# Performance work log

Measured on AMD Instinct MI355X. Metric: run time of the kernel, lower is better.

The kernel has to match this reference:

```python
import jax, jax.numpy as jnp
import numpy as np

EMBED_DIM = 256
MIN_SCALE = 0.5
BASE = 100.0
NDIM = 3
EPS = 1e-5


def basis_norm(psi, w):
    # w: [B, N] float weights; reduce over token dim (-2)
    norm_sq = jnp.sum(w[..., None] * (psi * psi), axis=-2, keepdims=True)
    return psi / jnp.sqrt(norm_sq + EPS)


def rotary(f, coords, lift):
    # lift: [D//2, 3]; phase: [B, N, D//2]
    phase = coords @ lift.T
    c, s = jnp.cos(phase), jnp.sin(phase)
    f1, f2 = jnp.split(f, 2, axis=-1)
    return jnp.concatenate([f1 * c - f2 * s, f1 * s + f2 * c], axis=-1)


def setup_inputs() -> dict:
    key = jax.random.key(0)
    ks = jax.random.split(key, 12)
    B, N, D = 4, 8192, EMBED_DIM
    phi = jax.random.normal(ks[0], (B, N, D), dtype=jnp.float32)
    coords = jax.random.normal(ks[1], (B, N, NDIM), dtype=jnp.float32)
    weights = jax.random.uniform(ks[2], (B, N), dtype=jnp.float32)
    scale = 1.0 / np.sqrt(D)
    Wq = jax.random.normal(ks[3], (D, D), dtype=jnp.float32) * scale
    bq = jnp.zeros((D,), dtype=jnp.float32)
    Wk = jax.random.normal(ks[4], (D, D), dtype=jnp.float32) * scale
    bk = jax.random.normal(ks[5], (D,), dtype=jnp.float32) * 0.01
    Wv = jax.random.normal(ks[6], (D, D), dtype=jnp.float32) * scale
    bv = jax.random.normal(ks[7], (D,), dtype=jnp.float32) * 0.01
    Wo = jax.random.normal(ks[8], (D, D), dtype=jnp.float32) * scale
    bo = jnp.zeros((D,), dtype=jnp.float32)
    # rotary lift init: k_norms * random unit vecs
    half = D // 2
    scales = BASE ** (-2.0 * np.arange(half) / D)
    k_norms = (2.0 * np.pi / MIN_SCALE) * scales  # [half]
    u = np.asarray(jax.random.normal(ks[9], (half, NDIM)))
    u = u / np.linalg.norm(u, axis=-1, keepdims=True)
    lift = jnp.asarray(k_norms[:, None] * u, dtype=jnp.float32)  # [half, 3]
    return {"phi": phi, "coords": coords, "weights": weights,
            "Wq": Wq, "bq": bq, "Wk": Wk, "bk": bk, "Wv": Wv, "bv": bv,
            "Wo": Wo, "bo": bo, "lift": lift}


def reference(phi, coords, weights, Wq, bq, Wk, bk, Wv, bv, Wo, bo, lift):
    q = phi @ Wq.T + bq
    k = basis_norm(phi @ Wk.T + bk, weights)
    v = basis_norm(phi @ Wv.T + bv, weights)
    q = rotary(q, coords, lift)
    k = rotary(k, coords, lift)
    k = k * weights[..., None]  # float-weights branch
    kv = jnp.einsum('bnd,bne->bde', k, v)   # [B, D, D]
    out = jnp.einsum('bnd,bde->bne', q, kv)  # [B, N, D]
    return out @ Wo.T + bo
```

## Files before the change

### kernel.cpp

```cpp
#include <hip/hip_runtime.h>
#include <hip/hip_bf16.h>
#include <stdint.h>

#define DEV __device__ __forceinline__

typedef short short8 __attribute__((ext_vector_type(8)));
typedef float floatx4 __attribute__((ext_vector_type(4)));
typedef uint32_t uint32x4 __attribute__((ext_vector_type(4)));

constexpr int D = 256;
constexpr int NTOK = 8192;
constexpr int MTOT = 4 * NTOK;

DEV void gl_lds16(const void* g, void* l) {
  __builtin_amdgcn_global_load_lds(
      (const __attribute__((address_space(1))) void*)g,
      (__attribute__((address_space(3))) void*)l, 16, 0, 0);
}

DEV float bflo(uint32_t u) { return __uint_as_float(u << 16); }
DEV float bfhi(uint32_t u) { return __uint_as_float(u & 0xffff0000u); }
DEV uint32_t packbf(float a, float b) {
  uint16_t xa = __builtin_bit_cast(uint16_t, __float2bfloat16(a));
  uint16_t xb = __builtin_bit_cast(uint16_t, __float2bfloat16(b));
  return (uint32_t)xa | ((uint32_t)xb << 16);
}

constexpr int PHI_E = MTOT * D;
constexpr int W_E = D * D;
__global__ __launch_bounds__(256) void convert(
    const float* __restrict__ phi, const float* __restrict__ Wq,
    const float* __restrict__ Wk, const float* __restrict__ Wv,
    uint32_t* __restrict__ dst, float2* __restrict__ nszero) {
  if (blockIdx.x == 0) {
    const float2 z = {0.f, 0.f};
#pragma unroll
    for (int k = 0; k < 4; k++) nszero[k * 256 + threadIdx.x] = z;
  }
  const int idx2 = blockIdx.x * 256 + threadIdx.x;
  const int e0 = idx2 * 2;
  float2 v;
  if (e0 < PHI_E) {
    v = ((const float2*)phi)[idx2];
  } else {
    int r = e0 - PHI_E;
    if (r < W_E) v = ((const float2*)Wq)[r >> 1];
    else if (r < 2 * W_E) v = ((const float2*)Wk)[(r - W_E) >> 1];
    else v = ((const float2*)Wv)[(r - 2 * W_E) >> 1];
  }
  dst[idx2] = packbf(v.x, v.y);
}

__global__ __launch_bounds__(256, 2) void gemm_qkv(
    const __hip_bfloat16* __restrict__ phi,
    const __hip_bfloat16* __restrict__ W16,
    const float* __restrict__ bq, const float* __restrict__ bk, const float* __restrict__ bv,
    const float* __restrict__ coords, const float* __restrict__ wts,
    const float* __restrict__ lift,
    __hip_bfloat16* __restrict__ Qb, __hip_bfloat16* __restrict__ Kb,
    __hip_bfloat16* __restrict__ Vb, float* __restrict__ nsk, float* __restrict__ nsv) {
  __shared__ __align__(16) char As[8192];
  __shared__ __align__(16) char Bs[16384];
  const int t = threadIdx.x, lane = t & 63, wid = t >> 6;
  const int wm = (wid & 1) * 64, wn = (wid >> 1) * 64;
  const int l16 = lane & 15, q4 = lane >> 4;
  const int m0 = blockIdx.x * 128;
  const int mat = blockIdx.y;
  const __hip_bfloat16* W = W16 + (size_t)mat * W_E;
  const float* bias = (mat == 0) ? bq : (mat == 1) ? bk : bv;
  __hip_bfloat16* Out = (mat == 0) ? Qb : (mat == 1) ? Kb : Vb;

  floatx4 acc[4][8] = {};

  const int srow = wid * 16 + (lane >> 2);
  const int skoff = (lane & 3) * 8;
  const __hip_bfloat16* gA = phi + (size_t)(m0 + srow) * D + skoff;
  const __hip_bfloat16* gB = W + (size_t)srow * D + skoff;
  char* lA = As + srow * 64 + skoff * 2;
  char* lB = Bs + srow * 64 + skoff * 2;

  for (int kt = 0; kt < 256; kt += 32) {
    gl_lds16(gA + kt, lA);
    gl_lds16(gA + kt + 64 * D, lA + 4096);
    gl_lds16(gB + kt, lB);
    gl_lds16(gB + kt + 64 * D, lB + 4096);
    gl_lds16(gB + kt + 128 * D, lB + 8192);
    gl_lds16(gB + kt + 192 * D, lB + 12288);
    __syncthreads();
    short8 af[4], bf8[8];
#pragma unroll
    for (int i = 0; i < 4; i++)
      af[i] = *(const short8*)(As + (wm + i * 16 + l16) * 64 + q4 * 16);
#pragma unroll
    for (int j = 0; j < 8; j++) {
      const int col = wn + (j & 3) * 16 + (j >> 2) * 128 + l16;
      bf8[j] = *(const short8*)(Bs + col * 64 + q4 * 16);
    }
#pragma unroll
    for (int i = 0; i < 4; i++)
#pragma unroll
      for (int j = 0; j < 8; j++)
        acc[i][j] = __builtin_amdgcn_mfma_f32_16x16x32_bf16(af[i], bf8[j], acc[i][j], 0, 0, 0);
    __syncthreads();
  }

  float bcol[8];
#pragma unroll
  for (int j = 0; j < 8; j++)
    bcol[j] = bias[wn + (j & 3) * 16 + (j >> 2) * 128 + l16];

  if (mat == 0) {
    float lx[4], ly[4], lz[4];
#pragma unroll
    for (int jj = 0; jj < 4; jj++) {
      const int c = wn + jj * 16 + l16;
      lx[jj] = lift[c * 3 + 0]; ly[jj] = lift[c * 3 + 1]; lz[jj] = lift[c * 3 + 2];
    }
#pragma unroll
    for (int i = 0; i < 4; i++) {
#pragma unroll
      for (int r = 0; r < 4; r++) {
        const int row = m0 + wm + i * 16 + q4 * 4 + r;
        const float cx = coords[row * 3 + 0];
        const float cy = coords[row * 3 + 1];
        const float cz = coords[row * 3 + 2];
#pragma unroll
        for (int jj = 0; jj < 4; jj++) {
          const int c = wn + jj * 16 + l16;
          const float p = cx * lx[jj] + cy * ly[jj] + cz * lz[jj];
          float s, cs;
          __sincosf(p, &s, &cs);
          const float f1 = acc[i][jj][r] + bcol[jj];
          const float f2 = acc[i][jj + 4][r] + bcol[jj + 4];
          Out[(size_t)row * D + c]       = __float2bfloat16(f1 * cs - f2 * s);
          Out[(size_t)row * D + c + 128] = __float2bfloat16(f1 * s + f2 * cs);
        }
      }
    }
  } else {
    const int b = m0 >> 13;
    float* ns = (mat == 1) ? nsk : nsv;
    float colsum[8] = {};
#pragma unroll
    for (int i = 0; i < 4; i++) {
#pragma unroll
      for (int r = 0; r < 4; r++) {
        const int row = m0 + wm + i * 16 + q4 * 4 + r;
        const float w = wts[row];
#pragma unroll
        for (int j = 0; j < 8; j++) {
          const int col = wn + (j & 3) * 16 + (j >> 2) * 128 + l16;
          const float psi = acc[i][j][r] + bcol[j];
          Out[(size_t)row * D + col] = __float2bfloat16(psi);
          colsum[j] += w * psi * psi;
        }
      }
    }
#pragma unroll
    for (int j = 0; j < 8; j++) {
      float s = colsum[j];
      s += __shfl_xor(s, 16);
      s += __shfl_xor(s, 32);
      if (q4 == 0) {
        const int col = wn + (j & 3) * 16 + (j >> 2) * 128 + l16;
        atomicAdd(&ns[b * D + col], s);
      }
    }
  }
}

__global__ __launch_bounds__(256, 2) void vproj_pk(
    const __hip_bfloat16* __restrict__ Vb, const float* __restrict__ Wo,
    const float* __restrict__ nsv, __hip_bfloat16* __restrict__ vproj,
    __hip_bfloat16* __restrict__ Kb, const float* __restrict__ coords,
    const float* __restrict__ wts, const float* __restrict__ lift,
    const float* __restrict__ nsk) {
  __shared__ __align__(16) char As[8192];
  __shared__ __align__(16) char Bs[8192];
  __shared__ __align__(16) float isv[256];
  const int bx = blockIdx.x;
  const int t = threadIdx.x;

  if (bx < 512) {
    const int lane = t & 63, wid = t >> 6;
    const int wm = (wid & 1) * 64, wn = (wid >> 1) * 64;
    const int l16 = lane & 15, q4 = lane >> 4;
    const int m0 = (bx >> 1) * 128, n0 = (bx & 1) * 128;
    const int b = m0 >> 13;
    isv[t] = rsqrtf(nsv[b * D + t] + 1e-5f);
    __syncthreads();
    floatx4 acc[4][4] = {};
    const int srow = wid * 16 + (lane >> 2);
    const int skoff = (lane & 3) * 8;
    const __hip_bfloat16* gA = Vb + (size_t)(m0 + srow) * D + skoff;
    const float* gB0 = Wo + (size_t)(n0 + srow) * D + skoff;
    const float* gB1 = Wo + (size_t)(n0 + srow + 64) * D + skoff;
    char* lA = As + srow * 64 + skoff * 2;
    char* lB = Bs + srow * 64 + skoff * 2;
    for (int kt = 0; kt < 256; kt += 32) {
      gl_lds16(gA + kt, lA);
      gl_lds16(gA + kt + 64 * D, lA + 4096);
      const float4 w0 = *(const float4*)(gB0 + kt);
      const float4 w1 = *(const float4*)(gB0 + kt + 4);
      const float4 w2 = *(const float4*)(gB1 + kt);
      const float4 w3 = *(const float4*)(gB1 + kt + 4);
      const float4 i0 = *(const float4*)(&isv[kt + skoff]);
      const float4 i1 = *(const float4*)(&isv[kt + skoff + 4]);
      uint32x4 p0, p1;
      p0[0] = packbf(w0.x * i0.x, w0.y * i0.y);
      p0[1] = packbf(w0.z * i0.z, w0.w * i0.w);
      p0[2] = packbf(w1.x * i1.x, w1.y * i1.y);
      p0[3] = packbf(w1.z * i1.z, w1.w * i1.w);
      p1[0] = packbf(w2.x * i0.x, w2.y * i0.y);
      p1[1] = packbf(w2.z * i0.z, w2.w * i0.w);
      p1[2] = packbf(w3.x * i1.x, w3.y * i1.y);
      p1[3] = packbf(w3.z * i1.z, w3.w * i1.w);
      *(uint32x4*)lB = p0;
      *(uint32x4*)(lB + 4096) = p1;
      __syncthreads();
      short8 af[4], bf8[4];
#pragma unroll
      for (int i = 0; i < 4; i++) {
        af[i]  = *(const short8*)(As + (wm + i * 16 + l16) * 64 + q4 * 16);
        bf8[i] = *(const short8*)(Bs + (wn + i * 16 + l16) * 64 + q4 * 16);
      }
#pragma unroll
      for (int i = 0; i < 4; i++)
#pragma unroll
        for (int j = 0; j < 4; j++)
          acc[i][j] = __builtin_amdgcn_mfma_f32_16x16x32_bf16(af[i], bf8[j], acc[i][j], 0, 0, 0);
      __syncthreads();
    }
#pragma unroll
    for (int j = 0; j < 4; j++) {
      const int colg = n0 + wn + j * 16 + l16;
#pragma unroll
      for (int i = 0; i < 4; i++) {
        const int rowg = m0 + wm + i * 16 + q4 * 4;
#pragma unroll
        for (int r = 0; r < 4; r++)
          vproj[(size_t)(rowg + r) * D + colg] = __float2bfloat16(acc[i][j][r]);
      }
    }
  } else {
    const int j = t & 63, rloc = t >> 6;
    const int pb = bx - 512;
    const int r0 = pb * 256;
    const int b = r0 >> 13;
    const int j0 = 2 * j, j1 = 2 * j + 1;
    const float lx0 = lift[j0 * 3 + 0], ly0 = lift[j0 * 3 + 1], lz0 = lift[j0 * 3 + 2];
    const float lx1 = lift[j1 * 3 + 0], ly1 = lift[j1 * 3 + 1], lz1 = lift[j1 * 3 + 2];
    const int nb = b * D;
    const float ik0 = rsqrtf(nsk[nb + j0] + 1e-5f);
    const float ik1 = rsqrtf(nsk[nb + j1] + 1e-5f);
    const float ik2 = rsqrtf(nsk[nb + 128 + j0] + 1e-5f);
    const float ik3 = rsqrtf(nsk[nb + 128 + j1] + 1e-5f);
    uint32_t* K32 = (uint32_t*)Kb;
    for (int it = 0; it < 64; it++) {
      const size_t row = (size_t)r0 + it * 4 + rloc;
      const float cx = coords[row * 3 + 0];
      const float cy = coords[row * 3 + 1];
      const float cz = coords[row * 3 + 2];
      const float p0 = cx * lx0 + cy * ly0 + cz * lz0;
      const float p1 = cx * lx1 + cy * ly1 + cz * lz1;
      float s0, c0, s1, c1;
      __sincosf(p0, &s0, &c0);
      __sincosf(p1, &s1, &c1);
      const float w = wts[row];
      const size_t base = row * 128;
      const uint32_t klo = K32[base + j], khi = K32[base + 64 + j];
      const float k1a = bflo(klo) * ik0, k1b = bfhi(klo) * ik1;
      const float k2a = bflo(khi) * ik2, k2b = bfhi(khi) * ik3;
      K32[base + j]      = packbf((k1a * c0 - k2a * s0) * w, (k1b * c1 - k2b * s1) * w);
      K32[base + 64 + j] = packbf((k1a * s0 + k2a * c0) * w, (k1b * s1 + k2b * c1) * w);
    }
  }
}

__global__ __launch_bounds__(256, 2) void gemm_tn(
    const __hip_bfloat16* __restrict__ Vp, const __hip_bfloat16* __restrict__ Kwb,
    __hip_bfloat16* __restrict__ part) {
  __shared__ __align__(16) char Asm[128 * 80];
  __shared__ __align__(16) char Bsm[128 * 80];
  const int t = threadIdx.x, lane = t & 63, wid = t >> 6;
  const int wm = (wid & 1) * 64, wn = (wid >> 1) * 64;
  const int l16 = lane & 15, q4 = lane >> 4;
  const int chunk = blockIdx.x, ed = blockIdx.y, b = blockIdx.z;
  const int e0 = (ed & 1) * 128, d0 = (ed >> 1) * 128;
  const uint32_t* V32 = (const uint32_t*)Vp;
  const uint32_t* K32 = (const uint32_t*)Kwb;
  const int s_np = (((t & 3) | ((t >> 6) << 2)) ^ ((t >> 4) & 3));
  const int s_e2lo = (t >> 2) & 15;
  floatx4 acc[4][4] = {};
  for (int nt = 0; nt < 256; nt += 32) {
    const int nbase = chunk * 256 + nt;
    const size_t tokbase = ((size_t)b * NTOK + nbase + 2 * s_np) * 128;
#pragma unroll
    for (int r = 0; r < 4; r++) {
      const int e2 = s_e2lo + r * 16;
      {
        const uint32_t a0 = V32[tokbase + (e0 >> 1) + e2];
        const uint32_t a1 = V32[tokbase + 128 + (e0 >> 1) + e2];
        *(uint32_t*)(Asm + (2 * e2) * 80 + 4 * s_np)     = (a0 & 0xffffu) | (a1 << 16);
        *(uint32_t*)(Asm + (2 * e2 + 1) * 80 + 4 * s_np) = (a0 >> 16) | (a1 & 0xffff0000u);
      }
      {
        const uint32_t b0 = K32[tokbase + (d0 >> 1) + e2];
        const uint32_t b1 = K32[tokbase + 128 + (d0 >> 1) + e2];
        *(uint32_t*)(Bsm + (2 * e2) * 80 + 4 * s_np)     = (b0 & 0xffffu) | (b1 << 16);
        *(uint32_t*)(Bsm + (2 * e2 + 1) * 80 + 4 * s_np) = (b0 >> 16) | (b1 & 0xffff0000u);
      }
    }
    __syncthreads();
    short8 af[4], bf8[4];
#pragma unroll
    for (int i = 0; i < 4; i++) {
      af[i]  = *(const short8*)(Asm + (wm + i * 16 + l16) * 80 + q4 * 16);
      bf8[i] = *(const short8*)(Bsm + (wn + i * 16 + l16) * 80 + q4 * 16);
    }
#pragma unroll
    for (int i = 0; i < 4; i++)
#pragma unroll
      for (int j = 0; j < 4; j++)
        acc[i][j] = __builtin_amdgcn_mfma_f32_16x16x32_bf16(af[i], bf8[j], acc[i][j], 0, 0, 0);
    __syncthreads();
  }
  __hip_bfloat16* pt = part + (((size_t)(chunk * 4 + b)) << 16);
#pragma unroll
  for (int i = 0; i < 4; i++) {
#pragma unroll
    for (int r = 0; r < 4; r++) {
      const int eg = e0 + wm + i * 16 + q4 * 4 + r;
#pragma unroll
      for (int j = 0; j < 4; j++) {
        const int dg = d0 + wn + j * 16 + l16;
        pt[eg * 256 + dg] = __float2bfloat16(acc[i][j][r]);
      }
    }
  }
}

__global__ __launch_bounds__(256) void reduce_kvt(const uint32_t* __restrict__ part,
                                                  uint32_t* __restrict__ P) {
  const int flat2 = blockIdx.x * 256 + threadIdx.x;
  const int b = flat2 >> 15;
  const int off = flat2 & 32767;
  float sx = 0, sy = 0;
#pragma unroll
  for (int c = 0; c < 32; c++) {
    const uint32_t u = part[(((size_t)(c * 4 + b)) << 15) + off];
    sx += bflo(u); sy += bfhi(u);
  }
  P[flat2] = packbf(sx, sy);
}

__global__ __launch_bounds__(256, 2) void gemm_out(
    const __hip_bfloat16* __restrict__ A, const __hip_bfloat16* __restrict__ Pm,
    const float* __restrict__ bo, float* __restrict__ Og) {
  __shared__ __align__(16) char As[8192];
  __shared__ __align__(16) char Bs[8192];
  const int t = threadIdx.x, lane = t & 63, wid = t >> 6;
  const int wm = (wid & 1) * 64, wn = (wid >> 1) * 64;
  const int l16 = lane & 15, q4 = lane >> 4;
  const int m0 = blockIdx.x * 128, n0 = blockIdx.y * 128;
  const int b = m0 >> 13;
  const __hip_bfloat16* W = Pm + ((size_t)b << 16);
  floatx4 acc[4][4] = {};
  const int srow = wid * 16 + (lane >> 2);
  const int skoff = (lane & 3) * 8;
  const __hip_bfloat16* gA = A + (size_t)(m0 + srow) * D + skoff;
  const __hip_bfloat16* gB = W + (size_t)(n0 + srow) * D + skoff;
  char* lA = As + srow * 64 + skoff * 2;
  char* lB = Bs + srow * 64 + skoff * 2;
  for (int kt = 0; kt < 256; kt += 32) {
    gl_lds16(gA + kt, lA);
    gl_lds16(gA + kt + 64 * D, lA + 4096);
    gl_lds16(gB + kt, lB);
    gl_lds16(gB + kt + 64 * D, lB + 4096);
    __syncthreads();
    short8 af[4], bf8[4];
#pragma unroll
    for (int i = 0; i < 4; i++) {
      af[i]  = *(const short8*)(As + (wm + i * 16 + l16) * 64 + q4 * 16);
      bf8[i] = *(const short8*)(Bs + (wn + i * 16 + l16) * 64 + q4 * 16);
    }
#pragma unroll
    for (int i = 0; i < 4; i++)
#pragma unroll
      for (int j = 0; j < 4; j++)
        acc[i][j] = __builtin_amdgcn_mfma_f32_16x16x32_bf16(af[i], bf8[j], acc[i][j], 0, 0, 0);
    __syncthreads();
  }
#pragma unroll
  for (int j = 0; j < 4; j++) {
    const int colg = n0 + wn + j * 16 + l16;
    const float bb = bo[colg];
#pragma unroll
    for (int i = 0; i < 4; i++) {
      const int rowg = m0 + wm + i * 16 + q4 * 4;
#pragma unroll
      for (int r = 0; r < 4; r++)
        Og[(size_t)(rowg + r) * D + colg] = acc[i][j][r] + bb;
    }
  }
}

extern "C" void kernel_launch(void* const* d_in, const int* in_sizes, int n_in,
                              void* d_out, int out_size, void* d_ws, size_t ws_size,
                              hipStream_t stream) {
  const float* phi    = (const float*)d_in[0];
  const float* coords = (const float*)d_in[1];
  const float* wts    = (const float*)d_in[2];
  const float* bq     = (const float*)d_in[4];
  const float* bk     = (const float*)d_in[6];
  const float* bv     = (const float*)d_in[8];
  const float* Wo     = (const float*)d_in[9];
  const float* bo     = (const float*)d_in[10];
  const float* lift   = (const float*)d_in[11];

  char* ws = (char*)d_ws;
  __hip_bfloat16* phi16 = (__hip_bfloat16*)ws;
  __hip_bfloat16* W16   = (__hip_bfloat16*)(ws + 16777216);
  const size_t QOFF = 17170432;
  const size_t SZ = (size_t)MTOT * D * 2;
  __hip_bfloat16* Qb = (__hip_bfloat16*)(ws + QOFF);
  __hip_bfloat16* Kb = (__hip_bfloat16*)(ws + QOFF + SZ);
  __hip_bfloat16* Vb = (__hip_bfloat16*)(ws + QOFF + 2 * SZ);
  const size_t NOFF = QOFF + 3 * SZ;
  float* nsk = (float*)(ws + NOFF);
  float* nsv = (float*)(ws + NOFF + 4096);
  __hip_bfloat16* part = (__hip_bfloat16*)(ws + NOFF + 8192);
  __hip_bfloat16* P = (__hip_bfloat16*)(ws + NOFF + 8192 + 16777216);
  __hip_bfloat16* vproj = (__hip_bfloat16*)(ws + NOFF + 8192 + 16777216 + 524288);

  convert<<<16768, 256, 0, stream>>>(phi, (const float*)d_in[3], (const float*)d_in[5],
                                     (const float*)d_in[7], (uint32_t*)ws, (float2*)(ws + NOFF));
  gemm_qkv<<<dim3(256, 3), 256, 0, stream>>>(phi16, W16, bq, bk, bv, coords, wts, lift,
                                             Qb, Kb, Vb, nsk, nsv);
  vproj_pk<<<640, 256, 0, stream>>>(Vb, Wo, nsv, vproj, Kb, coords, wts, lift, nsk);
  gemm_tn<<<dim3(32, 4, 4), 256, 0, stream>>>(vproj, Kb, part);
  reduce_kvt<<<512, 256, 0, stream>>>((const uint32_t*)part, (uint32_t*)P);
  gemm_out<<<dim3(256, 2), 256, 0, stream>>>(Qb, P, bo, (float*)d_out);
}
```

Before: 191.6 us.

## Reassociate Wo into small per-batch KV matrix instead of projecting V per token

Drops the per-token V·Wo projection over all 32K tokens and instead computes the 256x256 KV matrix from raw V, folding the V normalisation into the reduction. A small per-batch GEMM then multiplies Wo into KV, and Wo is converted to bf16 in the existing convert kernel. The K rotary pass becomes its own kernel, and the qkv and tn GEMMs remap block IDs to group blocks across XCDs. This removes a large token-dimension GEMM in exchange for one extra tiny launch and a different rounding order.

```diff
diff --git a/kernel.cpp b/kernel.cpp
--- a/kernel.cpp
+++ b/kernel.cpp
@@ -6,7 +6,6 @@
 
 typedef short short8 __attribute__((ext_vector_type(8)));
 typedef float floatx4 __attribute__((ext_vector_type(4)));
-typedef uint32_t uint32x4 __attribute__((ext_vector_type(4)));
 
 constexpr int D = 256;
 constexpr int NTOK = 8192;
@@ -31,6 +30,7 @@
 __global__ __launch_bounds__(256) void convert(
     const float* __restrict__ phi, const float* __restrict__ Wq,
     const float* __restrict__ Wk, const float* __restrict__ Wv,
+    const float* __restrict__ Wo,
     uint32_t* __restrict__ dst, float2* __restrict__ nszero) {
   if (blockIdx.x == 0) {
     const float2 z = {0.f, 0.f};
@@ -46,7 +46,8 @@
     int r = e0 - PHI_E;
     if (r < W_E) v = ((const float2*)Wq)[r >> 1];
     else if (r < 2 * W_E) v = ((const float2*)Wk)[(r - W_E) >> 1];
-    else v = ((const float2*)Wv)[(r - 2 * W_E) >> 1];
+    else if (r < 3 * W_E) v = ((const float2*)Wv)[(r - 2 * W_E) >> 1];
+    else v = ((const float2*)Wo)[(r - 3 * W_E) >> 1];
   }
   dst[idx2] = packbf(v.x, v.y);
 }
@@ -64,8 +65,10 @@
   const int t = threadIdx.x, lane = t & 63, wid = t >> 6;
   const int wm = (wid & 1) * 64, wn = (wid >> 1) * 64;
   const int l16 = lane & 15, q4 = lane >> 4;
-  const int m0 = blockIdx.x * 128;
-  const int mat = blockIdx.y;
+  const int bid = blockIdx.x;
+  const int g = (bid & 7) * 96 + (bid >> 3);
+  const int mat = g % 3;
+  const int m0 = (g / 3) * 128;
   const __hip_bfloat16* W = W16 + (size_t)mat * W_E;
   const float* bias = (mat == 0) ? bq : (mat == 1) ? bk : bv;
   __hip_bfloat16* Out = (mat == 0) ? Qb : (mat == 1) ? Kb : Vb;
@@ -169,126 +172,58 @@
   }
 }
 
-__global__ __launch_bounds__(256, 2) void vproj_pk(
-    const __hip_bfloat16* __restrict__ Vb, const float* __restrict__ Wo,
-    const float* __restrict__ nsv, __hip_bfloat16* __restrict__ vproj,
+__global__ __launch_bounds__(256) void kpoint(
     __hip_bfloat16* __restrict__ Kb, const float* __restrict__ coords,
     const float* __restrict__ wts, const float* __restrict__ lift,
     const float* __restrict__ nsk) {
-  __shared__ __align__(16) char As[8192];
-  __shared__ __align__(16) char Bs[8192];
-  __shared__ __align__(16) float isv[256];
-  const int bx = blockIdx.x;
   const int t = threadIdx.x;
-
-  if (bx < 512) {
-    const int lane = t & 63, wid = t >> 6;
-    const int wm = (wid & 1) * 64, wn = (wid >> 1) * 64;
-    const int l16 = lane & 15, q4 = lane >> 4;
-    const int m0 = (bx >> 1) * 128, n0 = (bx & 1) * 128;
-    const int b = m0 >> 13;
-    isv[t] = rsqrtf(nsv[b * D + t] + 1e-5f);
-    __syncthreads();
-    floatx4 acc[4][4] = {};
-    const int srow = wid * 16 + (lane >> 2);
-    const int skoff = (lane & 3) * 8;
-    const __hip_bfloat16* gA = Vb + (size_t)(m0 + srow) * D + skoff;
-    const float* gB0 = Wo + (size_t)(n0 + srow) * D + skoff;
-    const float* gB1 = Wo + (size_t)(n0 + srow + 64) * D + skoff;
-    char* lA = As + srow * 64 + skoff * 2;
-    char* lB = Bs + srow * 64 + skoff * 2;
-    for (int kt = 0; kt < 256; kt += 32) {
-      gl_lds16(gA + kt, lA);
-      gl_lds16(gA + kt + 64 * D, lA + 4096);
-      const float4 w0 = *(const float4*)(gB0 + kt);
-      const float4 w1 = *(const float4*)(gB0 + kt + 4);
-      const float4 w2 = *(const float4*)(gB1 + kt);
-      const float4 w3 = *(const float4*)(gB1 + kt + 4);
-      const float4 i0 = *(const float4*)(&isv[kt + skoff]);
-      const float4 i1 = *(const float4*)(&isv[kt + skoff + 4]);
-      uint32x4 p0, p1;
-      p0[0] = packbf(w0.x * i0.x, w0.y * i0.y);
-      p0[1] = packbf(w0.z * i0.z, w0.w * i0.w);
-      p0[2] = packbf(w1.x * i1.x, w1.y * i1.y);
-      p0[3] = packbf(w1.z * i1.z, w1.w * i1.w);
-      p1[0] = packbf(w2.x * i0.x, w2.y * i0.y);
-      p1[1] = packbf(w2.z * i0.z, w2.w * i0.w);
-      p1[2] = packbf(w3.x * i1.x, w3.y * i1.y);
-      p1[3] = packbf(w3.z * i1.z, w3.w * i1.w);
-      *(uint32x4*)lB = p0;
-      *(uint32x4*)(lB + 4096) = p1;
-      __syncthreads();
-      short8 af[4], bf8[4];
-#pragma unroll
-      for (int i = 0; i < 4; i++) {
-        af[i]  = *(const short8*)(As + (wm + i * 16 + l16) * 64 + q4 * 16);
-        bf8[i] = *(const short8*)(Bs + (wn + i * 16 + l16) * 64 + q4 * 16);
-      }
-#pragma unroll
-      for (int i = 0; i < 4; i++)
-#pragma unroll
-        for (int j = 0; j < 4; j++)
-          acc[i][j] = __builtin_amdgcn_mfma_f32_16x16x32_bf16(af[i], bf8[j], acc[i][j], 0, 0, 0);
-      __syncthreads();
-    }
-#pragma unroll
-    for (int j = 0; j < 4; j++) {
-      const int colg = n0 + wn + j * 16 + l16;
-#pragma unroll
-      for (int i = 0; i < 4; i++) {
-        const int rowg = m0 + wm + i * 16 + q4 * 4;
-#pragma unroll
-        for (int r = 0; r < 4; r++)
-          vproj[(size_t)(rowg + r) * D + colg] = __float2bfloat16(acc[i][j][r]);
-      }
-    }
-  } else {
-    const int j = t & 63, rloc = t >> 6;
-    const int pb = bx - 512;
-    const int r0 = pb * 256;
-    const int b = r0 >> 13;
-    const int j0 = 2 * j, j1 = 2 * j + 1;
-    const float lx0 = lift[j0 * 3 + 0], ly0 = lift[j0 * 3 + 1], lz0 = lift[j0 * 3 + 2];
-    const float lx1 = lift[j1 * 3 + 0], ly1 = lift[j1 * 3 + 1], lz1 = lift[j1 * 3 + 2];
-    const int nb = b * D;
-    const float ik0 = rsqrtf(nsk[nb + j0] + 1e-5f);
-    const float ik1 = rsqrtf(nsk[nb + j1] + 1e-5f);
-    const float ik2 = rsqrtf(nsk[nb + 128 + j0] + 1e-5f);
-    const float ik3 = rsqrtf(nsk[nb + 128 + j1] + 1e-5f);
-    uint32_t* K32 = (uint32_t*)Kb;
-    for (int it = 0; it < 64; it++) {
-      const size_t row = (size_t)r0 + it * 4 + rloc;
-      const float cx = coords[row * 3 + 0];
-      const float cy = coords[row * 3 + 1];
-      const float cz = coords[row * 3 + 2];
-      const float p0 = cx * lx0 + cy * ly0 + cz * lz0;
-      const float p1 = cx * lx1 + cy * ly1 + cz * lz1;
-      float s0, c0, s1, c1;
-      __sincosf(p0, &s0, &c0);
-      __sincosf(p1, &s1, &c1);
-      const float w = wts[row];
-      const size_t base = row * 128;
-      const uint32_t klo = K32[base + j], khi = K32[base + 64 + j];
-      const float k1a = bflo(klo) * ik0, k1b = bfhi(klo) * ik1;
-      const float k2a = bflo(khi) * ik2, k2b = bfhi(khi) * ik3;
-      K32[base + j]      = packbf((k1a * c0 - k2a * s0) * w, (k1b * c1 - k2b * s1) * w);
-      K32[base + 64 + j] = packbf((k1a * s0 + k2a * c0) * w, (k1b * s1 + k2b * c1) * w);
-    }
+  const int j = t & 63, rloc = t >> 6;
+  const int r0 = blockIdx.x * 128;
+  const int b = r0 >> 13;
+  const int j0 = 2 * j, j1 = 2 * j + 1;
+  const float lx0 = lift[j0 * 3 + 0], ly0 = lift[j0 * 3 + 1], lz0 = lift[j0 * 3 + 2];
+  const float lx1 = lift[j1 * 3 + 0], ly1 = lift[j1 * 3 + 1], lz1 = lift[j1 * 3 + 2];
+  const int nb = b * D;
+  const float ik0 = rsqrtf(nsk[nb + j0] + 1e-5f);
+  const float ik1 = rsqrtf(nsk[nb + j1] + 1e-5f);
+  const float ik2 = rsqrtf(nsk[nb + 128 + j0] + 1e-5f);
+  const float ik3 = rsqrtf(nsk[nb + 128 + j1] + 1e-5f);
+  uint32_t* K32 = (uint32_t*)Kb;
+  for (int it = 0; it < 32; it++) {
+    const size_t row = (size_t)r0 + it * 4 + rloc;
+    const float cx = coords[row * 3 + 0];
+    const float cy = coords[row * 3 + 1];
+    const float cz = coords[row * 3 + 2];
+    const float p0 = cx * lx0 + cy * ly0 + cz * lz0;
+    const float p1 = cx * lx1 + cy * ly1 + cz * lz1;
+    float s0, c0, s1, c1;
+    __sincosf(p0, &s0, &c0);
+    __sincosf(p1, &s1, &c1);
+    const float w = wts[row];
+    const size_t base = row * 128;
+    const uint32_t klo = K32[base + j], khi = K32[base + 64 + j];
+    const float k1a = bflo(klo) * ik0, k1b = bfhi(klo) * ik1;
+    const float k2a = bflo(khi) * ik2, k2b = bfhi(khi) * ik3;
+    K32[base + j]      = packbf((k1a * c0 - k2a * s0) * w, (k1b * c1 - k2b * s1) * w);
+    K32[base + 64 + j] = packbf((k1a * s0 + k2a * c0) * w, (k1b * s1 + k2b * c1) * w);
   }
 }
 
 __global__ __launch_bounds__(256, 2) void gemm_tn(
-    const __hip_bfloat16* __restrict__ Vp, const __hip_bfloat16* __restrict__ Kwb,
+    const __hip_bfloat16* __restrict__ Kwb, const __hip_bfloat16* __restrict__ Vb,
     __hip_bfloat16* __restrict__ part) {
   __shared__ __align__(16) char Asm[128 * 80];
   __shared__ __align__(16) char Bsm[128 * 80];
   const int t = threadIdx.x, lane = t & 63, wid = t >> 6;
   const int wm = (wid & 1) * 64, wn = (wid >> 1) * 64;
   const int l16 = lane & 15, q4 = lane >> 4;
-  const int chunk = blockIdx.x, ed = blockIdx.y, b = blockIdx.z;
+  const int bid = blockIdx.x;
+  const int g = (bid & 7) * 64 + (bid >> 3);
+  const int ed = g & 3, rest = g >> 2;
+  const int chunk = rest & 31, b = rest >> 5;
   const int e0 = (ed & 1) * 128, d0 = (ed >> 1) * 128;
-  const uint32_t* V32 = (const uint32_t*)Vp;
-  const uint32_t* K32 = (const uint32_t*)Kwb;
+  const uint32_t* A32 = (const uint32_t*)Kwb;
+  const uint32_t* B32 = (const uint32_t*)Vb;
   const int s_np = (((t & 3) | ((t >> 6) << 2)) ^ ((t >> 4) & 3));
   const int s_e2lo = (t >> 2) & 15;
   floatx4 acc[4][4] = {};
@@ -299,14 +234,14 @@
     for (int r = 0; r < 4; r++) {
       const int e2 = s_e2lo + r * 16;
       {
-        const uint32_t a0 = V32[tokbase + (e0 >> 1) + e2];
-        const uint32_t a1 = V32[tokbase + 128 + (e0 >> 1) + e2];
+        const uint32_t a0 = A32[tokbase + (d0 >> 1) + e2];
+        const uint32_t a1 = A32[tokbase + 128 + (d0 >> 1) + e2];
         *(uint32_t*)(Asm + (2 * e2) * 80 + 4 * s_np)     = (a0 & 0xffffu) | (a1 << 16);
         *(uint32_t*)(Asm + (2 * e2 + 1) * 80 + 4 * s_np) = (a0 >> 16) | (a1 & 0xffff0000u);
       }
       {
-        const uint32_t b0 = K32[tokbase + (d0 >> 1) + e2];
-        const uint32_t b1 = K32[tokbase + 128 + (d0 >> 1) + e2];
+        const uint32_t b0 = B32[tokbase + (e0 >> 1) + e2];
+        const uint32_t b1 = B32[tokbase + 128 + (e0 >> 1) + e2];
         *(uint32_t*)(Bsm + (2 * e2) * 80 + 4 * s_np)     = (b0 & 0xffffu) | (b1 << 16);
         *(uint32_t*)(Bsm + (2 * e2 + 1) * 80 + 4 * s_np) = (b0 >> 16) | (b1 & 0xffff0000u);
       }
@@ -330,28 +265,82 @@
   for (int i = 0; i < 4; i++) {
 #pragma unroll
     for (int r = 0; r < 4; r++) {
-      const int eg = e0 + wm + i * 16 + q4 * 4 + r;
+      const int rg = d0 + wm + i * 16 + q4 * 4 + r;
 #pragma unroll
       for (int j = 0; j < 4; j++) {
-        const int dg = d0 + wn + j * 16 + l16;
-        pt[eg * 256 + dg] = __float2bfloat16(acc[i][j][r]);
+        const int cg = e0 + wn + j * 16 + l16;
+        pt[rg * 256 + cg] = __float2bfloat16(acc[i][j][r]);
       }
     }
   }
 }
 
 __global__ __launch_bounds__(256) void reduce_kvt(const uint32_t* __restrict__ part,
-                                                  uint32_t* __restrict__ P) {
+                                                  uint32_t* __restrict__ Ps,
+                                                  const float* __restrict__ nsv) {
   const int flat2 = blockIdx.x * 256 + threadIdx.x;
   const int b = flat2 >> 15;
   const int off = flat2 & 32767;
+  const int es = (off & 127) * 2;
   float sx = 0, sy = 0;
 #pragma unroll
   for (int c = 0; c < 32; c++) {
     const uint32_t u = part[(((size_t)(c * 4 + b)) << 15) + off];
     sx += bflo(u); sy += bfhi(u);
   }
-  P[flat2] = packbf(sx, sy);
+  const float iv0 = rsqrtf(nsv[b * D + es] + 1e-5f);
+  const float iv1 = rsqrtf(nsv[b * D + es + 1] + 1e-5f);
+  Ps[flat2] = packbf(sx * iv0, sy * iv1);
+}
+
+__global__ __launch_bounds__(256, 2) void gemm_mt(
+    const __hip_bfloat16* __restrict__ Wo16, const __hip_bfloat16* __restrict__ Ps,
+    __hip_bfloat16* __restrict__ MT) {
+  __shared__ __align__(16) char As[8192];
+  __shared__ __align__(16) char Bs[8192];
+  const int t = threadIdx.x, lane = t & 63, wid = t >> 6;
+  const int wm = (wid & 1) * 64, wn = (wid >> 1) * 64;
+  const int l16 = lane & 15, q4 = lane >> 4;
+  const int m0 = blockIdx.x * 128, n0 = blockIdx.y * 128, b = blockIdx.z;
+  const __hip_bfloat16* Bm = Ps + ((size_t)b << 16);
+  floatx4 acc[4][4] = {};
+  const int srow = wid * 16 + (lane >> 2);
+  const int skoff = (lane & 3) * 8;
+  const __hip_bfloat16* gA = Wo16 + (size_t)(m0 + srow) * D + skoff;
+  const __hip_bfloat16* gB = Bm + (size_t)(n0 + srow) * D + skoff;
+  char* lA = As + srow * 64 + skoff * 2;
+  char* lB = Bs + srow * 64 + skoff * 2;
+  for (int kt = 0; kt < 256; kt += 32) {
+    gl_lds16(gA + kt, lA);
+    gl_lds16(gA + kt + 64 * D, lA + 4096);
+    gl_lds16(gB + kt, lB);
+    gl_lds16(gB + kt + 64 * D, lB + 4096);
+    __syncthreads();
+    short8 af[4], bf8[4];
+#pragma unroll
+    for (int i = 0; i < 4; i++) {
+      af[i]  = *(const short8*)(As + (wm + i * 16 + l16) * 64 + q4 * 16);
+      bf8[i] = *(const short8*)(Bs + (wn + i * 16 + l16) * 64 + q4 * 16);
+    }
+#pragma unroll
+    for (int i = 0; i < 4; i++)
+#pragma unroll
+      for (int j = 0; j < 4; j++)
+        acc[i][j] = __builtin_amdgcn_mfma_f32_16x16x32_bf16(af[i], bf8[j], acc[i][j], 0, 0, 0);
+    __syncthreads();
+  }
+  __hip_bfloat16* Ob = MT + ((size_t)b << 16);
+#pragma unroll
+  for (int j = 0; j < 4; j++) {
+    const int colg = n0 + wn + j * 16 + l16;
+#pragma unroll
+    for (int i = 0; i < 4; i++) {
+      const int rowg = m0 + wm + i * 16 + q4 * 4;
+#pragma unroll
+      for (int r = 0; r < 4; r++)
+        Ob[(size_t)(rowg + r) * D + colg] = __float2bfloat16(acc[i][j][r]);
+    }
+  }
 }
 
 __global__ __launch_bounds__(256, 2) void gemm_out(
@@ -421,7 +410,7 @@
   char* ws = (char*)d_ws;
   __hip_bfloat16* phi16 = (__hip_bfloat16*)ws;
   __hip_bfloat16* W16   = (__hip_bfloat16*)(ws + 16777216);
-  const size_t QOFF = 17170432;
+  const size_t QOFF = 17301504;
   const size_t SZ = (size_t)MTOT * D * 2;
   __hip_bfloat16* Qb = (__hip_bfloat16*)(ws + QOFF);
   __hip_bfloat16* Kb = (__hip_bfloat16*)(ws + QOFF + SZ);
@@ -430,15 +419,17 @@
   float* nsk = (float*)(ws + NOFF);
   float* nsv = (float*)(ws + NOFF + 4096);
   __hip_bfloat16* part = (__hip_bfloat16*)(ws + NOFF + 8192);
-  __hip_bfloat16* P = (__hip_bfloat16*)(ws + NOFF + 8192 + 16777216);
-  __hip_bfloat16* vproj = (__hip_bfloat16*)(ws + NOFF + 8192 + 16777216 + 524288);
-
-  convert<<<16768, 256, 0, stream>>>(phi, (const float*)d_in[3], (const float*)d_in[5],
-                                     (const float*)d_in[7], (uint32_t*)ws, (float2*)(ws + NOFF));
-  gemm_qkv<<<dim3(256, 3), 256, 0, stream>>>(phi16, W16, bq, bk, bv, coords, wts, lift,
-                                             Qb, Kb, Vb, nsk, nsv);
-  vproj_pk<<<640, 256, 0, stream>>>(Vb, Wo, nsv, vproj, Kb, coords, wts, lift, nsk);
-  gemm_tn<<<dim3(32, 4, 4), 256, 0, stream>>>(vproj, Kb, part);
-  reduce_kvt<<<512, 256, 0, stream>>>((const uint32_t*)part, (uint32_t*)P);
-  gemm_out<<<dim3(256, 2), 256, 0, stream>>>(Qb, P, bo, (float*)d_out);
-}
+  __hip_bfloat16* Ps   = (__hip_bfloat16*)(ws + NOFF + 8192 + 16777216);
+  __hip_bfloat16* MT   = (__hip_bfloat16*)(ws + NOFF + 8192 + 16777216 + 524288);
+
+  convert<<<16896, 256, 0, stream>>>(phi, (const float*)d_in[3], (const float*)d_in[5],
+                                     (const float*)d_in[7], Wo,
+                                     (uint32_t*)ws, (float2*)(ws + NOFF));
+  gemm_qkv<<<768, 256, 0, stream>>>(phi16, W16, bq, bk, bv, coords, wts, lift,
+                                    Qb, Kb, Vb, nsk, nsv);
+  kpoint<<<256, 256, 0, stream>>>(Kb, coords, wts, lift, nsk);
+  gemm_tn<<<512, 256, 0, stream>>>(Kb, Vb, part);
+  reduce_kvt<<<512, 256, 0, stream>>>((const uint32_t*)part, (uint32_t*)Ps, nsv);
+  gemm_mt<<<dim3(2, 2, 4), 256, 0, stream>>>(W16 + 3 * W_E, Ps, MT);
+  gemm_out<<<dim3(256, 2), 256, 0, stream>>>(Qb, MT, bo, (float*)d_out);
+}
```

Result: faster. 180.9 us (-5.6%).
